# Kernel optimization log

Hardware: AMD Instinct MI355X
Metric: run time of the kernel (lower is better)

Reference implementation:

```python
import jax, jax.numpy as jnp
import numpy as np

# static degree histogram (degrees 0..10), atoms sorted by degree as in DeepChem ConvMol
COUNTS = [1024, 24576, 36864, 36864, 20480, 2048, 512, 256, 128, 64, 64]
OFFS = np.cumsum([0] + COUNTS)
N_ATOMS = int(OFFS[-1])  # 122880
BATCH = 4096
F_IN = 75
HID = 64
MAXDEG = 10
EPS = 1e-3  # keras BatchNormalization default epsilon


def _graph_conv(atoms, adjs, W, b):
    # W: [2*MAXDEG+1, F, HID]; order: (rel, self) per degree 1..10, then degree 0
    outs = []
    for d in range(1, MAXDEG + 1):
        self_a = atoms[OFFS[d]:OFFS[d + 1]]              # [n_d, F]
        rel = atoms[adjs[d - 1]].sum(axis=1)             # gather [n_d, d, F] -> sum neighbors
        outs.append(rel @ W[2 * (d - 1)] + b[2 * (d - 1)]
                    + self_a @ W[2 * d - 1] + b[2 * d - 1])
    out0 = atoms[OFFS[0]:OFFS[1]] @ W[2 * MAXDEG] + b[2 * MAXDEG]
    return jnp.tanh(jnp.concatenate([out0] + outs, axis=0))


def _graph_pool(atoms, adjs):
    outs = [atoms[OFFS[0]:OFFS[1]]]  # degree-0 atoms pass through
    for d in range(1, MAXDEG + 1):
        self_a = atoms[OFFS[d]:OFFS[d + 1]][:, None, :]  # [n_d, 1, F]
        gathered = atoms[adjs[d - 1]]                    # [n_d, d, F]
        outs.append(jnp.max(jnp.concatenate([self_a, gathered], axis=1), axis=1))
    return jnp.concatenate(outs, axis=0)


def _bn(x, g, beta, mean, var):
    return g * (x - mean) * jax.lax.rsqrt(var + EPS) + beta


def setup_inputs():
    key = jax.random.key(0)
    ks = jax.random.split(key, 20)
    inp = {}
    inp["atoms"] = jax.random.normal(ks[0], (N_ATOMS, F_IN), jnp.float32)
    inp["membership"] = jax.random.randint(ks[1], (N_ATOMS,), 0, BATCH, jnp.int32)
    for d in range(1, MAXDEG + 1):
        inp[f"adj{d}"] = jax.random.randint(ks[1 + d], (COUNTS[d], d), 0, N_ATOMS, jnp.int32)
    inp["x_add"] = jax.random.normal(ks[12], (BATCH, 15), jnp.float32)
    w = lambda k, s: jax.random.normal(k, s, jnp.float32) * 0.05
    inp["gc1_W"] = w(ks[13], (2 * MAXDEG + 1, F_IN, HID))
    inp["gc1_b"] = jnp.zeros((2 * MAXDEG + 1, HID), jnp.float32)
    inp["gc2_W"] = w(ks[14], (2 * MAXDEG + 1, HID, HID))
    inp["gc2_b"] = jnp.zeros((2 * MAXDEG + 1, HID), jnp.float32)
    inp["bn1_gamma"] = jnp.ones((HID,), jnp.float32)
    inp["bn1_beta"] = jnp.zeros((HID,), jnp.float32)
    inp["bn1_mean"] = jnp.zeros((HID,), jnp.float32)
    inp["bn1_var"] = jnp.ones((HID,), jnp.float32)
    inp["bn3_gamma"] = jnp.ones((128,), jnp.float32)
    inp["bn3_beta"] = jnp.zeros((128,), jnp.float32)
    inp["bn3_mean"] = jnp.zeros((128,), jnp.float32)
    inp["bn3_var"] = jnp.ones((128,), jnp.float32)
    inp["d1_W"] = w(ks[15], (HID, 128))
    inp["d1_b"] = jnp.zeros((128,), jnp.float32)
    inp["d2_W"] = w(ks[16], (256, 1))
    inp["d2_b"] = jnp.zeros((1,), jnp.float32)
    inp["d3_W"] = jnp.array([0.5, -1, -1, 1, 1, 1, 1, 1, -1, -1, -1, -1, -1, -1, -1, -1],
                              jnp.float32).reshape(16, 1)
    inp["d3_b"] = jnp.zeros((1,), jnp.float32)
    return inp


def reference(atoms, membership, adj1, adj2, adj3, adj4, adj5, adj6, adj7, adj8, adj9, adj10,
              x_add, gc1_W, gc1_b, gc2_W, gc2_b,
              bn1_gamma, bn1_beta, bn1_mean, bn1_var,
              bn3_gamma, bn3_beta, bn3_mean, bn3_var,
              d1_W, d1_b, d2_W, d2_b, d3_W, d3_b):
    adjs = [adj1, adj2, adj3, adj4, adj5, adj6, adj7, adj8, adj9, adj10]
    h = _graph_conv(atoms, adjs, gc1_W, gc1_b)
    h = _bn(h, bn1_gamma, bn1_beta, bn1_mean, bn1_var)
    h = _graph_pool(h, adjs)
    h = _graph_conv(h, adjs, gc2_W, gc2_b)
    # NOTE: source model reuses batch_norm1 here (bug in original); replicated faithfully
    h = _bn(h, bn1_gamma, bn1_beta, bn1_mean, bn1_var)
    h = _graph_pool(h, adjs)
    h = jnp.tanh(h @ d1_W + d1_b)
    h = _bn(h, bn3_gamma, bn3_beta, bn3_mean, bn3_var)
    # GraphGather: per-molecule sum and max readout
    s = jax.ops.segment_sum(h, membership, num_segments=BATCH)
    m = jax.ops.segment_max(h, membership, num_segments=BATCH)
    mol = jnp.tanh(jnp.concatenate([s, m], axis=1))      # [BATCH, 256]
    model_var = mol @ d2_W + d2_b                          # [BATCH, 1]
    binding = jnp.concatenate([model_var, x_add], axis=1)  # [BATCH, 16]
    return binding @ d3_W + d3_b                           # [BATCH, 1]
```

## Files before the change

kernel.cpp:

```cpp
#include <hip/hip_runtime.h>
#include <math.h>

#define NATOMS 122880
#define BATCH 4096
#define EPS 1e-3f

__constant__ int d_OFFS[12] = {0,1024,25600,62464,99328,119808,121856,122368,122624,122752,122816,122880};
__constant__ int d_TCUM[12] = {0,32,800,1952,3104,3744,3808,3824,3832,3836,3838,3840};

struct Adj { const int* p[10]; };

typedef __attribute__((ext_vector_type(8))) short bf16x8;
typedef __attribute__((ext_vector_type(4))) float f32x4;

__device__ inline float bf2f(ushort u) { return __uint_as_float(((unsigned)u) << 16); }
__device__ inline ushort f2bf(float f) {
    unsigned u = __float_as_uint(f);
    return (ushort)((u + 0x7fffu + ((u >> 16) & 1u)) >> 16);
}

__device__ inline float fast_tanh(float x) {
    float e = __builtin_amdgcn_exp2f(x * 2.8853900817779268f);
    return 1.f - 2.f * __builtin_amdgcn_rcpf(e + 1.f);
}

__global__ __launch_bounds__(256)
void prep_kernel(const float* __restrict__ x, ushort* __restrict__ xb,
                 const float* __restrict__ W1, const float* __restrict__ W2,
                 const float* __restrict__ W3,
                 ushort* __restrict__ Wt1, ushort* __restrict__ Wt2,
                 ushort* __restrict__ Wt3, int* __restrict__ hist)
{
    __shared__ float s_row[2400];
    const int tid = threadIdx.x;
    const int bx  = blockIdx.x;
    if (bx < 3840) {
        const size_t base = (size_t)bx * 32;
        for (int e = tid; e < 2400; e += 256) s_row[e] = x[base * 75 + e];
        __syncthreads();
        for (int e = tid; e < 320; e += 256) {
            int a = e / 10, ch = e - a * 10;
            unsigned px[4];
            #pragma unroll
            for (int q = 0; q < 4; ++q) {
                int k0 = ch * 8 + q * 2, k1 = k0 + 1;
                float v0 = (k0 < 75) ? s_row[a * 75 + k0] : 0.f;
                float v1 = (k1 < 75) ? s_row[a * 75 + k1] : 0.f;
                px[q] = (unsigned)f2bf(v0) | ((unsigned)f2bf(v1) << 16);
            }
            uint4 pv; pv.x = px[0]; pv.y = px[1]; pv.z = px[2]; pv.w = px[3];
            *(uint4*)(xb + (base + a) * 80 + ch * 8) = pv;
        }
    } else if (bx < 4664) {
        int idx = (bx - 3840) * 256 + tid;
        if (idx < 112640) {
            int m = idx / 10240;
            int rem = idx - m * 10240;
            int n = rem / 160, k = rem - n * 160;
            float v = 0.f;
            if (k < 80) {
                if (k < 75) v = (m == 0) ? 0.f : W1[(size_t)(2*m-2)*75*64 + k*64 + n];
            } else {
                int kk = k - 80;
                if (kk < 75) v = (m == 0) ? W1[(size_t)20*75*64 + kk*64 + n]
                                          : W1[(size_t)(2*m-1)*75*64 + kk*64 + n];
            }
            Wt1[(size_t)m*10240 + n*160 + k] = f2bf(v);
        } else if (idx < 202752) {
            int i2 = idx - 112640;
            int m = i2 / 8192;
            int rem = i2 - m * 8192;
            int n = rem / 128, k = rem - n * 128;
            float v;
            if (k < 64) v = (m == 0) ? 0.f : W2[(size_t)(2*m-2)*64*64 + k*64 + n];
            else        v = (m == 0) ? W2[(size_t)20*64*64 + (k-64)*64 + n]
                                     : W2[(size_t)(2*m-1)*64*64 + (k-64)*64 + n];
            Wt2[(size_t)m*8192 + n*128 + k] = f2bf(v);
        } else {
            int i3 = idx - 202752;
            int n = i3 >> 6, k = i3 & 63;
            Wt3[(size_t)n*64 + k] = f2bf(W3[(size_t)k*128 + n]);
        }
    } else {
        hist[(bx - 4664) * 256 + tid] = 0;
    }
}

__global__ __launch_bounds__(256)
void hist_kernel(const int* __restrict__ mem, int* __restrict__ hist) {
    int i = blockIdx.x * 256 + threadIdx.x;
    atomicAdd(&hist[mem[i]], 1);
}

__global__ __launch_bounds__(1024)
void scan_kernel(const int* __restrict__ hist, int* __restrict__ cursor) {
    __shared__ int s_sums[16];
    const int t = threadIdx.x;
    const int lane = t & 63, wid = t >> 6;
    int4 v = ((const int4*)hist)[t];
    int tot = v.x + v.y + v.z + v.w;
    int x = tot;
    #pragma unroll
    for (int o = 1; o < 64; o <<= 1) { int y = __shfl_up(x, o); if (lane >= o) x += y; }
    if (lane == 63) s_sums[wid] = x;
    __syncthreads();
    if (wid == 0) {
        int y = (lane < 16) ? s_sums[lane] : 0;
        #pragma unroll
        for (int o = 1; o < 16; o <<= 1) { int z = __shfl_up(y, o); if (lane >= o) y += z; }
        if (lane < 16) s_sums[lane] = y;
    }
    __syncthreads();
    int base = (wid > 0 ? s_sums[wid - 1] : 0) + (x - tot);
    int4 c;
    c.x = base; c.y = base + v.x; c.z = base + v.x + v.y; c.w = base + v.x + v.y + v.z;
    ((int4*)cursor)[t] = c;
}

__global__ __launch_bounds__(256)
void scatter_kernel(const int* __restrict__ mem, int* __restrict__ cursor,
                    int* __restrict__ sidx) {
    int i = blockIdx.x * 256 + threadIdx.x;
    int m = mem[i];
    int p = atomicAdd(&cursor[m], 1);
    sidx[p] = i;
}


template<int FP, int KPAD, int D>
__device__ inline void stage_rows_v2(ushort (*s_A)[KPAD], const int* __restrict__ s_adj,
                                     const ushort* __restrict__ xb, int row0, int tid)
{
    constexpr int NCH = FP / 8;
    for (int e = tid; e < 32 * NCH; e += 256) {
        const int a = e / NCH, ch = e - a * NCH;
        const int co = ch * 8;
        uint4 sv = *(const uint4*)(xb + (size_t)(row0 + a) * FP + co);
        float acc[8] = {0.f,0.f,0.f,0.f,0.f,0.f,0.f,0.f};
        #pragma unroll
        for (int j = 0; j < D; ++j) {
            uint4 nv = *(const uint4*)(xb + (size_t)s_adj[a * D + j] * FP + co);
            unsigned u[4] = {nv.x, nv.y, nv.z, nv.w};
            #pragma unroll
            for (int q = 0; q < 4; ++q) {
                acc[2*q]   += __uint_as_float(u[q] << 16);
                acc[2*q+1] += __uint_as_float(u[q] & 0xFFFF0000u);
            }
        }
        unsigned pz[4];
        #pragma unroll
        for (int q = 0; q < 4; ++q)
            pz[q] = (unsigned)f2bf(acc[2*q]) | ((unsigned)f2bf(acc[2*q+1]) << 16);
        uint4 rv; rv.x = pz[0]; rv.y = pz[1]; rv.z = pz[2]; rv.w = pz[3];
        *(uint4*)&s_A[a][co] = rv;
        *(uint4*)&s_A[a][FP + co] = sv;
    }
}

template<int FP, int KTOT, int KPAD>
__global__ __launch_bounds__(256)
void conv_mfma(const ushort* __restrict__ xb, const ushort* __restrict__ Wt,
               const float* __restrict__ b,
               const float* __restrict__ g, const float* __restrict__ beta,
               const float* __restrict__ mean, const float* __restrict__ var,
               Adj adj, ushort* __restrict__ out)
{
    __shared__ ushort s_A[32][KPAD];
    __shared__ int s_adj[320];

    const int tid = threadIdx.x;
    const int bx  = blockIdx.x;
    int d = 0;
    #pragma unroll
    for (int i = 1; i <= 10; ++i) if (bx >= d_TCUM[i]) d = i;
    const int tile = bx - d_TCUM[d];
    const int row0 = d_OFFS[d] + tile * 32;

    if (d > 0) {
        const int* ap = adj.p[d-1] + (size_t)tile * 32 * d;
        for (int e = tid; e < 32 * d; e += 256) s_adj[e] = ap[e];
    }
    __syncthreads();

    switch (d) {
        case 0:  stage_rows_v2<FP,KPAD,0 >(s_A, s_adj, xb, row0, tid); break;
        case 1:  stage_rows_v2<FP,KPAD,1 >(s_A, s_adj, xb, row0, tid); break;
        case 2:  stage_rows_v2<FP,KPAD,2 >(s_A, s_adj, xb, row0, tid); break;
        case 3:  stage_rows_v2<FP,KPAD,3 >(s_A, s_adj, xb, row0, tid); break;
        case 4:  stage_rows_v2<FP,KPAD,4 >(s_A, s_adj, xb, row0, tid); break;
        case 5:  stage_rows_v2<FP,KPAD,5 >(s_A, s_adj, xb, row0, tid); break;
        case 6:  stage_rows_v2<FP,KPAD,6 >(s_A, s_adj, xb, row0, tid); break;
        case 7:  stage_rows_v2<FP,KPAD,7 >(s_A, s_adj, xb, row0, tid); break;
        case 8:  stage_rows_v2<FP,KPAD,8 >(s_A, s_adj, xb, row0, tid); break;
        case 9:  stage_rows_v2<FP,KPAD,9 >(s_A, s_adj, xb, row0, tid); break;
        default: stage_rows_v2<FP,KPAD,10>(s_A, s_adj, xb, row0, tid); break;
    }
    __syncthreads();

    const int w = tid >> 6, lane = tid & 63;
    const int r = w & 1, c = w >> 1;
    const int l15 = lane & 15, lg = lane >> 4;
    const int kgrp = lg * 8;

    f32x4 acc0 = {}, acc1 = {};
    const ushort* ap0 = &s_A[r * 16 + l15][kgrp];
    const ushort* wt0 = Wt + ((size_t)d * 64 + c * 32 + l15) * KTOT + kgrp;
    const ushort* wt1 = wt0 + 16 * KTOT;
    #pragma unroll
    for (int ks = 0; ks < KTOT / 32; ++ks) {
        bf16x8 af = *(const bf16x8*)(ap0 + ks * 32);
        bf16x8 b0 = *(const bf16x8*)(wt0 + ks * 32);
        bf16x8 b1 = *(const bf16x8*)(wt1 + ks * 32);
        acc0 = __builtin_amdgcn_mfma_f32_16x16x32_bf16(af, b0, acc0, 0, 0, 0);
        acc1 = __builtin_amdgcn_mfma_f32_16x16x32_bf16(af, b1, acc1, 0, 0, 0);
    }

    const int col0 = c * 32 + l15;
    const int col1 = col0 + 16;
    float bias0, bias1;
    if (d > 0) {
        bias0 = b[(2*d-2)*64 + col0] + b[(2*d-1)*64 + col0];
        bias1 = b[(2*d-2)*64 + col1] + b[(2*d-1)*64 + col1];
    } else {
        bias0 = b[20*64 + col0];
        bias1 = b[20*64 + col1];
    }
    const float g0 = g[col0], be0 = beta[col0], m0 = mean[col0], r0 = rsqrtf(var[col0] + EPS);
    const float g1 = g[col1], be1 = beta[col1], m1 = mean[col1], r1 = rsqrtf(var[col1] + EPS);
    const int rbase = row0 + r * 16 + lg * 4;
    #pragma unroll
    for (int i = 0; i < 4; ++i) {
        float t0 = fast_tanh(acc0[i] + bias0);
        float t1 = fast_tanh(acc1[i] + bias1);
        out[(size_t)(rbase + i) * 64 + col0] = f2bf(g0 * (t0 - m0) * r0 + be0);
        out[(size_t)(rbase + i) * 64 + col1] = f2bf(g1 * (t1 - m1) * r1 + be1);
    }
}


template<int D>
__device__ inline void pool_body(const ushort* __restrict__ h, ushort* __restrict__ out,
                                 const int* __restrict__ s_adj, int row0, int tid)
{
    const int a = tid >> 3, co = (tid & 7) * 8;
    uint4 sv = *(const uint4*)(h + (size_t)(row0 + a) * 64 + co);
    unsigned su[4] = {sv.x, sv.y, sv.z, sv.w};
    float mx[8];
    #pragma unroll
    for (int q = 0; q < 4; ++q) {
        mx[2*q]   = __uint_as_float(su[q] << 16);
        mx[2*q+1] = __uint_as_float(su[q] & 0xFFFF0000u);
    }
    #pragma unroll
    for (int j = 0; j < D; ++j) {
        uint4 nv = *(const uint4*)(h + (size_t)s_adj[a * D + j] * 64 + co);
        unsigned u[4] = {nv.x, nv.y, nv.z, nv.w};
        #pragma unroll
        for (int q = 0; q < 4; ++q) {
            mx[2*q]   = fmaxf(mx[2*q],   __uint_as_float(u[q] << 16));
            mx[2*q+1] = fmaxf(mx[2*q+1], __uint_as_float(u[q] & 0xFFFF0000u));
        }
    }
    unsigned pz[4];
    #pragma unroll
    for (int q = 0; q < 4; ++q)
        pz[q] = (__float_as_uint(mx[2*q]) >> 16) | (__float_as_uint(mx[2*q+1]) & 0xFFFF0000u);
    uint4 pv; pv.x = pz[0]; pv.y = pz[1]; pv.z = pz[2]; pv.w = pz[3];
    *(uint4*)(out + (size_t)(row0 + a) * 64 + co) = pv;
}

__global__ __launch_bounds__(256)
void pool_tile(const ushort* __restrict__ h, ushort* __restrict__ out, Adj adj)
{
    __shared__ int s_adj[320];
    const int tid = threadIdx.x;
    const int bx  = blockIdx.x;
    int d = 0;
    #pragma unroll
    for (int i = 1; i <= 10; ++i) if (bx >= d_TCUM[i]) d = i;
    const int tile = bx - d_TCUM[d];
    const int row0 = d_OFFS[d] + tile * 32;

    if (d > 0) {
        const int* ap = adj.p[d-1] + (size_t)tile * 32 * d;
        for (int e = tid; e < 32 * d; e += 256) s_adj[e] = ap[e];
        __syncthreads();
    }
    switch (d) {
        case 0:  pool_body<0 >(h, out, s_adj, row0, tid); break;
        case 1:  pool_body<1 >(h, out, s_adj, row0, tid); break;
        case 2:  pool_body<2 >(h, out, s_adj, row0, tid); break;
        case 3:  pool_body<3 >(h, out, s_adj, row0, tid); break;
        case 4:  pool_body<4 >(h, out, s_adj, row0, tid); break;
        case 5:  pool_body<5 >(h, out, s_adj, row0, tid); break;
        case 6:  pool_body<6 >(h, out, s_adj, row0, tid); break;
        case 7:  pool_body<7 >(h, out, s_adj, row0, tid); break;
        case 8:  pool_body<8 >(h, out, s_adj, row0, tid); break;
        case 9:  pool_body<9 >(h, out, s_adj, row0, tid); break;
        default: pool_body<10>(h, out, s_adj, row0, tid); break;
    }
}

__global__ __launch_bounds__(256)
void dense_seg_fused(const ushort* __restrict__ h, const ushort* __restrict__ Wt3,
                     const float* __restrict__ b,
                     const float* __restrict__ g3, const float* __restrict__ b3,
                     const float* __restrict__ m3, const float* __restrict__ v3,
                     const int* __restrict__ sidx,
                     const int* __restrict__ hist, const int* __restrict__ endc,
                     const float* __restrict__ x_add,
                     const float* __restrict__ d2W, const float* __restrict__ d2b,
                     const float* __restrict__ d3W, const float* __restrict__ d3b,
                     float* __restrict__ out)
{
    __shared__ ushort s_x[32][72];
    __shared__ float s_sum[4][64];
    __shared__ float s_max[4][64];
    __shared__ float s_red[4];

    const int mol = blockIdx.x;
    const int cnt = hist[mol];
    const int start = endc[mol] - cnt;

    const int tid = threadIdx.x;
    const int w = tid >> 6, lane = tid & 63;
    const int r = w & 1, cb = (w >> 1) * 64;
    const int l15 = lane & 15, lg = lane >> 4;

    int   col[4];
    float bias[4], gg[4], bb[4], mm[4], rr[4];
    #pragma unroll
    for (int j = 0; j < 4; ++j) {
        col[j]  = cb + j * 16 + l15;
        bias[j] = b[col[j]];
        gg[j] = g3[col[j]]; bb[j] = b3[col[j]]; mm[j] = m3[col[j]];
        rr[j] = rsqrtf(v3[col[j]] + EPS);
    }

    const float NEGINF = __int_as_float(0xFF800000);
    float rsum[4] = {0.f, 0.f, 0.f, 0.f};
    float rmax[4] = {NEGINF, NEGINF, NEGINF, NEGINF};

    const int a = tid >> 3, part = tid & 7;
    for (int base = 0; base < cnt; base += 32) {
        uint4 val = {0u, 0u, 0u, 0u};
        int ri = base + a;
        if (ri < cnt) {
            int row = sidx[start + ri];
            val = *(const uint4*)(h + (size_t)row * 64 + part * 8);
        }
        *(uint4*)&s_x[a][part * 8] = val;
        __syncthreads();

        f32x4 acc[4] = {};
        const ushort* ap0 = &s_x[r * 16 + l15][lg * 8];
        #pragma unroll
        for (int ks = 0; ks < 2; ++ks) {
            bf16x8 af = *(const bf16x8*)(ap0 + ks * 32);
            #pragma unroll
            for (int j = 0; j < 4; ++j) {
                const ushort* wt = Wt3 + (size_t)col[j] * 64 + lg * 8 + ks * 32;
                bf16x8 bv = *(const bf16x8*)wt;
                acc[j] = __builtin_amdgcn_mfma_f32_16x16x32_bf16(af, bv, acc[j], 0, 0, 0);
            }
        }

        const int rowbase = base + r * 16 + lg * 4;
        #pragma unroll
        for (int i = 0; i < 4; ++i) {
            if (rowbase + i < cnt) {
                #pragma unroll
                for (int j = 0; j < 4; ++j) {
                    float hv = gg[j] * (fast_tanh(acc[j][i] + bias[j]) - mm[j]) * rr[j] + bb[j];
                    rsum[j] += hv;
                    rmax[j] = fmaxf(rmax[j], hv);
                }
            }
        }
        __syncthreads();
    }

    #pragma unroll
    for (int j = 0; j < 4; ++j) {
        rsum[j] += __shfl_xor(rsum[j], 16);
        rsum[j] += __shfl_xor(rsum[j], 32);
        rmax[j] = fmaxf(rmax[j], __shfl_xor(rmax[j], 16));
        rmax[j] = fmaxf(rmax[j], __shfl_xor(rmax[j], 32));
    }
    if (lane < 16) {
        #pragma unroll
        for (int j = 0; j < 4; ++j) {
            s_sum[w][j * 16 + lane] = rsum[j];
            s_max[w][j * 16 + lane] = rmax[j];
        }
    }
    __syncthreads();

    {
        const int part2 = tid >> 7;
        const int c  = tid & 127;
        const int ch = c >> 6, cc = c & 63;
        float val;
        if (part2 == 0) val = s_sum[2*ch][cc] + s_sum[2*ch + 1][cc];
        else            val = fmaxf(s_max[2*ch][cc], s_max[2*ch + 1][cc]);
        float p = fast_tanh(val) * d2W[part2 * 128 + c];
        #pragma unroll
        for (int o = 32; o > 0; o >>= 1) p += __shfl_down(p, o);
        if (lane == 0) s_red[w] = p;
    }
    __syncthreads();
    if (tid == 0) {
        float mv = s_red[0] + s_red[1] + s_red[2] + s_red[3] + d2b[0];
        float rv = mv * d3W[0] + d3b[0];
        for (int i = 0; i < 15; ++i) rv += x_add[(size_t)mol * 15 + i] * d3W[1 + i];
        out[mol] = rv;
    }
}

extern "C" void kernel_launch(void* const* d_in, const int* in_sizes, int n_in,
                              void* d_out, int out_size, void* d_ws, size_t ws_size,
                              hipStream_t stream) {
    const float* atoms      = (const float*)d_in[0];
    const int*   membership = (const int*)  d_in[1];
    Adj adj;
    for (int i = 0; i < 10; ++i) adj.p[i] = (const int*)d_in[2 + i];
    const float* x_add = (const float*)d_in[12];
    const float* gc1_W = (const float*)d_in[13];
    const float* gc1_b = (const float*)d_in[14];
    const float* gc2_W = (const float*)d_in[15];
    const float* gc2_b = (const float*)d_in[16];
    const float* bn1_g = (const float*)d_in[17];
    const float* bn1_b = (const float*)d_in[18];
    const float* bn1_m = (const float*)d_in[19];
    const float* bn1_v = (const float*)d_in[20];
    const float* bn3_g = (const float*)d_in[21];
    const float* bn3_b = (const float*)d_in[22];
    const float* bn3_m = (const float*)d_in[23];
    const float* bn3_v = (const float*)d_in[24];
    const float* d1_W  = (const float*)d_in[25];
    const float* d1_b  = (const float*)d_in[26];
    const float* d2_W  = (const float*)d_in[27];
    const float* d2_b  = (const float*)d_in[28];
    const float* d3_W  = (const float*)d_in[29];
    const float* d3_b  = (const float*)d_in[30];
    float* out = (float*)d_out;

    ushort* xb  = (ushort*)d_ws;
    ushort* hA  = xb  + (size_t)9830400;
    ushort* hB  = hA  + (size_t)7864320;
    ushort* Wt1 = hB  + (size_t)7864320;
    ushort* Wt2 = Wt1 + (size_t)112640;
    ushort* Wt3 = Wt2 + (size_t)90112;
    int*   sidx = (int*)(Wt3 + (size_t)8192);
    int*   hist = sidx + NATOMS;
    int* cursor = hist + BATCH;

    prep_kernel<<<4680, 256, 0, stream>>>(atoms, xb, gc1_W, gc2_W, d1_W,
                                          Wt1, Wt2, Wt3, hist);
    hist_kernel<<<480, 256, 0, stream>>>(membership, hist);
    scan_kernel<<<1, 1024, 0, stream>>>(hist, cursor);
    scatter_kernel<<<480, 256, 0, stream>>>(membership, cursor, sidx);

    conv_mfma<80,160,168><<<3840, 256, 0, stream>>>(xb, Wt1, gc1_b,
                                                    bn1_g, bn1_b, bn1_m, bn1_v, adj, hA);
    pool_tile<<<3840, 256, 0, stream>>>(hA, hB, adj);
    conv_mfma<64,128,136><<<3840, 256, 0, stream>>>(hB, Wt2, gc2_b,
                                                    bn1_g, bn1_b, bn1_m, bn1_v, adj, hA);
    pool_tile<<<3840, 256, 0, stream>>>(hA, hB, adj);
    dense_seg_fused<<<BATCH, 256, 0, stream>>>(hB, Wt3, d1_b,
                                               bn3_g, bn3_b, bn3_m, bn3_v,
                                               sidx, hist, cursor,
                                               x_add, d2_W, d2_b, d3_W, d3_b, out);
}
```

Measured before the change: 149.2 us.

## Fuse second graph pool into dense/segment readout via flattened edge list

Removes the second pool_tile launch and computes the neighbor max-pool on the fly inside dense_seg_fused, gathering each atom's neighbors from the conv output through a flattened edge array. The edge array is built by extra blocks added to prep_kernel, which copy all per-degree adjacency lists into one contiguous buffer. This saves a kernel launch and a full write and read of the pooled activation tensor. In exchange, the readout kernel now does dependent, uncoalesced neighbor gathers per atom with a variable-length loop, so its own runtime grows.

```diff
diff --git a/kernel.cpp b/kernel.cpp
--- a/kernel.cpp
+++ b/kernel.cpp
@@ -7,6 +7,8 @@
 
 __constant__ int d_OFFS[12] = {0,1024,25600,62464,99328,119808,121856,122368,122624,122752,122816,122880};
 __constant__ int d_TCUM[12] = {0,32,800,1952,3104,3744,3808,3824,3832,3836,3838,3840};
+__constant__ int d_ECUM[11] = {0,24576,98304,208896,290816,301056,304128,305920,306944,307520,308160};
+__constant__ int d_ETC[11] = {0,96,384,816,1136,1176,1188,1195,1199,1202,1205};
 
 struct Adj { const int* p[10]; };
 
@@ -29,7 +31,8 @@
                  const float* __restrict__ W1, const float* __restrict__ W2,
                  const float* __restrict__ W3,
                  ushort* __restrict__ Wt1, ushort* __restrict__ Wt2,
-                 ushort* __restrict__ Wt3, int* __restrict__ hist)
+                 ushort* __restrict__ Wt3, int* __restrict__ hist,
+                 Adj adj, int* __restrict__ edges)
 {
     __shared__ float s_row[2400];
     const int tid = threadIdx.x;
@@ -81,8 +84,16 @@
             int n = i3 >> 6, k = i3 & 63;
             Wt3[(size_t)n*64 + k] = f2bf(W3[(size_t)k*128 + n]);
         }
+    } else if (bx < 4680) {
+        hist[(bx - 4664) * 256 + tid] = 0;
     } else {
-        hist[(bx - 4664) * 256 + tid] = 0;
+        int eb = bx - 4680;
+        int d = 1;
+        #pragma unroll
+        for (int i = 1; i <= 9; ++i) if (eb >= d_ETC[i]) d = i + 1;
+        int pos = (eb - d_ETC[d-1]) * 256 + tid;
+        int ecnt = d_ECUM[d] - d_ECUM[d-1];
+        if (pos < ecnt) edges[d_ECUM[d-1] + pos] = adj.p[d-1][pos];
     }
 }
 
@@ -302,12 +313,13 @@
 }
 
 __global__ __launch_bounds__(256)
-void dense_seg_fused(const ushort* __restrict__ h, const ushort* __restrict__ Wt3,
+void dense_seg_fused(const ushort* __restrict__ hA, const ushort* __restrict__ Wt3,
                      const float* __restrict__ b,
                      const float* __restrict__ g3, const float* __restrict__ b3,
                      const float* __restrict__ m3, const float* __restrict__ v3,
                      const int* __restrict__ sidx,
                      const int* __restrict__ hist, const int* __restrict__ endc,
+                     const int* __restrict__ edges,
                      const float* __restrict__ x_add,
                      const float* __restrict__ d2W, const float* __restrict__ d2b,
                      const float* __restrict__ d3W, const float* __restrict__ d3b,
@@ -341,15 +353,43 @@
     float rsum[4] = {0.f, 0.f, 0.f, 0.f};
     float rmax[4] = {NEGINF, NEGINF, NEGINF, NEGINF};
 
-    const int a = tid >> 3, part = tid & 7;
+    const int a = tid >> 3, co = (tid & 7) * 8;
     for (int base = 0; base < cnt; base += 32) {
         uint4 val = {0u, 0u, 0u, 0u};
         int ri = base + a;
         if (ri < cnt) {
             int row = sidx[start + ri];
-            val = *(const uint4*)(h + (size_t)row * 64 + part * 8);
-        }
-        *(uint4*)&s_x[a][part * 8] = val;
+            uint4 sv = *(const uint4*)(hA + (size_t)row * 64 + co);
+            unsigned su[4] = {sv.x, sv.y, sv.z, sv.w};
+            float mx[8];
+            #pragma unroll
+            for (int q = 0; q < 4; ++q) {
+                mx[2*q]   = __uint_as_float(su[q] << 16);
+                mx[2*q+1] = __uint_as_float(su[q] & 0xFFFF0000u);
+            }
+            int d = 0;
+            #pragma unroll
+            for (int i = 1; i <= 10; ++i) if (row >= d_OFFS[i]) d = i;
+            if (d > 0) {
+                int estart = d_ECUM[d-1] + (row - d_OFFS[d]) * d;
+                for (int j = 0; j < d; ++j) {
+                    int nr = edges[estart + j];
+                    uint4 nv = *(const uint4*)(hA + (size_t)nr * 64 + co);
+                    unsigned u[4] = {nv.x, nv.y, nv.z, nv.w};
+                    #pragma unroll
+                    for (int q = 0; q < 4; ++q) {
+                        mx[2*q]   = fmaxf(mx[2*q],   __uint_as_float(u[q] << 16));
+                        mx[2*q+1] = fmaxf(mx[2*q+1], __uint_as_float(u[q] & 0xFFFF0000u));
+                    }
+                }
+            }
+            unsigned pz[4];
+            #pragma unroll
+            for (int q = 0; q < 4; ++q)
+                pz[q] = (__float_as_uint(mx[2*q]) >> 16) | (__float_as_uint(mx[2*q+1]) & 0xFFFF0000u);
+            val.x = pz[0]; val.y = pz[1]; val.z = pz[2]; val.w = pz[3];
+        }
+        *(uint4*)&s_x[a][co] = val;
         __syncthreads();
 
         f32x4 acc[4] = {};
@@ -454,9 +494,10 @@
     int*   sidx = (int*)(Wt3 + (size_t)8192);
     int*   hist = sidx + NATOMS;
     int* cursor = hist + BATCH;
-
-    prep_kernel<<<4680, 256, 0, stream>>>(atoms, xb, gc1_W, gc2_W, d1_W,
-                                          Wt1, Wt2, Wt3, hist);
+    int*  edges = cursor + BATCH;
+
+    prep_kernel<<<5885, 256, 0, stream>>>(atoms, xb, gc1_W, gc2_W, d1_W,
+                                          Wt1, Wt2, Wt3, hist, adj, edges);
     hist_kernel<<<480, 256, 0, stream>>>(membership, hist);
     scan_kernel<<<1, 1024, 0, stream>>>(hist, cursor);
     scatter_kernel<<<480, 256, 0, stream>>>(membership, cursor, sidx);
@@ -466,9 +507,8 @@
     pool_tile<<<3840, 256, 0, stream>>>(hA, hB, adj);
     conv_mfma<64,128,136><<<3840, 256, 0, stream>>>(hB, Wt2, gc2_b,
                                                     bn1_g, bn1_b, bn1_m, bn1_v, adj, hA);
-    pool_tile<<<3840, 256, 0, stream>>>(hA, hB, adj);
-    dense_seg_fused<<<BATCH, 256, 0, stream>>>(hB, Wt3, d1_b,
+    dense_seg_fused<<<BATCH, 256, 0, stream>>>(hA, Wt3, d1_b,
                                                bn3_g, bn3_b, bn3_m, bn3_v,
-                                               sidx, hist, cursor,
+                                               sidx, hist, cursor, edges,
                                                x_add, d2_W, d2_b, d3_W, d3_b, out);
 }
```

Result: slower. 159.5 us (+6.9%).

## Process one molecule per wavefront in dense+segment readout kernel

Applied to the files above, without the earlier changes.

The final dense+gather kernel now gives each wavefront its own molecule, with four molecules per block, where before a full 256-thread block handled one molecule. Each wave covers all 128 output columns over 16-row tiles held in its own LDS slice, so block-wide __syncthreads and the cross-wave shared reductions go away. The aim is to cut barrier overhead and idle threads for small molecules (about 30 atoms on average). In exchange each wave carries more registers (8 accumulators) and does the row work serially.

```diff
diff --git a/kernel.cpp b/kernel.cpp
--- a/kernel.cpp
+++ b/kernel.cpp
@@ -302,115 +302,99 @@
 }
 
 __global__ __launch_bounds__(256)
-void dense_seg_fused(const ushort* __restrict__ h, const ushort* __restrict__ Wt3,
-                     const float* __restrict__ b,
-                     const float* __restrict__ g3, const float* __restrict__ b3,
-                     const float* __restrict__ m3, const float* __restrict__ v3,
-                     const int* __restrict__ sidx,
-                     const int* __restrict__ hist, const int* __restrict__ endc,
-                     const float* __restrict__ x_add,
-                     const float* __restrict__ d2W, const float* __restrict__ d2b,
-                     const float* __restrict__ d3W, const float* __restrict__ d3b,
-                     float* __restrict__ out)
-{
-    __shared__ ushort s_x[32][72];
-    __shared__ float s_sum[4][64];
-    __shared__ float s_max[4][64];
-    __shared__ float s_red[4];
-
-    const int mol = blockIdx.x;
+void dense_seg_wave(const ushort* __restrict__ h, const ushort* __restrict__ Wt3,
+                    const float* __restrict__ b,
+                    const float* __restrict__ g3, const float* __restrict__ b3,
+                    const float* __restrict__ m3, const float* __restrict__ v3,
+                    const int* __restrict__ sidx,
+                    const int* __restrict__ hist, const int* __restrict__ endc,
+                    const float* __restrict__ x_add,
+                    const float* __restrict__ d2W, const float* __restrict__ d2b,
+                    const float* __restrict__ d3W, const float* __restrict__ d3b,
+                    float* __restrict__ out)
+{
+    __shared__ ushort s_x[4][16][72];
+    const int tid = threadIdx.x;
+    const int w = tid >> 6, lane = tid & 63;
+    const int mol = blockIdx.x * 4 + w;
     const int cnt = hist[mol];
     const int start = endc[mol] - cnt;
-
-    const int tid = threadIdx.x;
-    const int w = tid >> 6, lane = tid & 63;
-    const int r = w & 1, cb = (w >> 1) * 64;
     const int l15 = lane & 15, lg = lane >> 4;
 
-    int   col[4];
-    float bias[4], gg[4], bb[4], mm[4], rr[4];
-    #pragma unroll
-    for (int j = 0; j < 4; ++j) {
-        col[j]  = cb + j * 16 + l15;
-        bias[j] = b[col[j]];
-        gg[j] = g3[col[j]]; bb[j] = b3[col[j]]; mm[j] = m3[col[j]];
-        rr[j] = rsqrtf(v3[col[j]] + EPS);
+    float bias[8], gg[8], bb[8], mm[8], rr[8];
+    #pragma unroll
+    for (int j = 0; j < 8; ++j) {
+        int c = j * 16 + l15;
+        bias[j] = b[c]; gg[j] = g3[c]; bb[j] = b3[c]; mm[j] = m3[c];
+        rr[j] = rsqrtf(v3[c] + EPS);
     }
 
     const float NEGINF = __int_as_float(0xFF800000);
-    float rsum[4] = {0.f, 0.f, 0.f, 0.f};
-    float rmax[4] = {NEGINF, NEGINF, NEGINF, NEGINF};
-
-    const int a = tid >> 3, part = tid & 7;
-    for (int base = 0; base < cnt; base += 32) {
-        uint4 val = {0u, 0u, 0u, 0u};
-        int ri = base + a;
-        if (ri < cnt) {
-            int row = sidx[start + ri];
-            val = *(const uint4*)(h + (size_t)row * 64 + part * 8);
-        }
-        *(uint4*)&s_x[a][part * 8] = val;
-        __syncthreads();
-
-        f32x4 acc[4] = {};
-        const ushort* ap0 = &s_x[r * 16 + l15][lg * 8];
+    float rsum[8] = {0.f,0.f,0.f,0.f,0.f,0.f,0.f,0.f};
+    float rmax[8] = {NEGINF,NEGINF,NEGINF,NEGINF,NEGINF,NEGINF,NEGINF,NEGINF};
+
+    for (int base = 0; base < cnt; base += 16) {
+        #pragma unroll
+        for (int p = 0; p < 2; ++p) {
+            int e = p * 64 + lane;
+            int row_i = e >> 3, part = e & 7;
+            uint4 val = {0u, 0u, 0u, 0u};
+            int ri = base + row_i;
+            if (ri < cnt) {
+                int row = sidx[start + ri];
+                val = *(const uint4*)(h + (size_t)row * 64 + part * 8);
+            }
+            *(uint4*)&s_x[w][row_i][part * 8] = val;
+        }
+        asm volatile("s_waitcnt lgkmcnt(0)" ::: "memory");
+
+        f32x4 acc[8] = {};
         #pragma unroll
         for (int ks = 0; ks < 2; ++ks) {
-            bf16x8 af = *(const bf16x8*)(ap0 + ks * 32);
+            bf16x8 af = *(const bf16x8*)&s_x[w][l15][lg * 8 + ks * 32];
             #pragma unroll
-            for (int j = 0; j < 4; ++j) {
-                const ushort* wt = Wt3 + (size_t)col[j] * 64 + lg * 8 + ks * 32;
+            for (int j = 0; j < 8; ++j) {
+                const ushort* wt = Wt3 + (size_t)(j * 16 + l15) * 64 + lg * 8 + ks * 32;
                 bf16x8 bv = *(const bf16x8*)wt;
                 acc[j] = __builtin_amdgcn_mfma_f32_16x16x32_bf16(af, bv, acc[j], 0, 0, 0);
             }
         }
 
-        const int rowbase = base + r * 16 + lg * 4;
         #pragma unroll
         for (int i = 0; i < 4; ++i) {
-            if (rowbase + i < cnt) {
+            int ri = base + lg * 4 + i;
+            if (ri < cnt) {
                 #pragma unroll
-                for (int j = 0; j < 4; ++j) {
+                for (int j = 0; j < 8; ++j) {
                     float hv = gg[j] * (fast_tanh(acc[j][i] + bias[j]) - mm[j]) * rr[j] + bb[j];
                     rsum[j] += hv;
                     rmax[j] = fmaxf(rmax[j], hv);
                 }
             }
         }
-        __syncthreads();
-    }
-
-    #pragma unroll
-    for (int j = 0; j < 4; ++j) {
+    }
+
+    #pragma unroll
+    for (int j = 0; j < 8; ++j) {
         rsum[j] += __shfl_xor(rsum[j], 16);
         rsum[j] += __shfl_xor(rsum[j], 32);
         rmax[j] = fmaxf(rmax[j], __shfl_xor(rmax[j], 16));
         rmax[j] = fmaxf(rmax[j], __shfl_xor(rmax[j], 32));
     }
-    if (lane < 16) {
-        #pragma unroll
-        for (int j = 0; j < 4; ++j) {
-            s_sum[w][j * 16 + lane] = rsum[j];
-            s_max[w][j * 16 + lane] = rmax[j];
-        }
-    }
-    __syncthreads();
-
-    {
-        const int part2 = tid >> 7;
-        const int c  = tid & 127;
-        const int ch = c >> 6, cc = c & 63;
-        float val;
-        if (part2 == 0) val = s_sum[2*ch][cc] + s_sum[2*ch + 1][cc];
-        else            val = fmaxf(s_max[2*ch][cc], s_max[2*ch + 1][cc]);
-        float p = fast_tanh(val) * d2W[part2 * 128 + c];
-        #pragma unroll
-        for (int o = 32; o > 0; o >>= 1) p += __shfl_down(p, o);
-        if (lane == 0) s_red[w] = p;
-    }
-    __syncthreads();
-    if (tid == 0) {
-        float mv = s_red[0] + s_red[1] + s_red[2] + s_red[3] + d2b[0];
+
+    float p = 0.f;
+    #pragma unroll
+    for (int j = 0; j < 8; ++j) {
+        int c = j * 16 + l15;
+        p += fast_tanh(rsum[j]) * d2W[c];
+        p += fast_tanh(rmax[j]) * d2W[128 + c];
+    }
+    p = (lane < 16) ? p : 0.f;
+    #pragma unroll
+    for (int o = 32; o > 0; o >>= 1) p += __shfl_down(p, o);
+
+    if (lane == 0) {
+        float mv = p + d2b[0];
         float rv = mv * d3W[0] + d3b[0];
         for (int i = 0; i < 15; ++i) rv += x_add[(size_t)mol * 15 + i] * d3W[1 + i];
         out[mol] = rv;
@@ -467,8 +451,8 @@
     conv_mfma<64,128,136><<<3840, 256, 0, stream>>>(hB, Wt2, gc2_b,
                                                     bn1_g, bn1_b, bn1_m, bn1_v, adj, hA);
     pool_tile<<<3840, 256, 0, stream>>>(hA, hB, adj);
-    dense_seg_fused<<<BATCH, 256, 0, stream>>>(hB, Wt3, d1_b,
-                                               bn3_g, bn3_b, bn3_m, bn3_v,
-                                               sidx, hist, cursor,
-                                               x_add, d2_W, d2_b, d3_W, d3_b, out);
-}
+    dense_seg_wave<<<1024, 256, 0, stream>>>(hB, Wt3, d1_b,
+                                             bn3_g, bn3_b, bn3_m, bn3_v,
+                                             sidx, hist, cursor,
+                                             x_add, d2_W, d2_b, d3_W, d3_b, out);
+}
```

Result: slower. 155.7 us (+4.4%).
